# Performance work log

Hardware: AMD Instinct MI355X
Metric: run time of the kernel (lower is better)

The kernel has to match this reference:

```python
import jax, jax.numpy as jnp
import numpy as np
import math

WH, WW = 8, 8
N = WH * WW            # tokens per window = 64
DIM = 128
H = 4                  # num_heads
HD = DIM // H          # head_dim = 32
B_ = 3072              # num_windows * batch
NW = 192               # windows per image (96/8 * 128/8)
LAMBDA_INIT = 0.8 - 0.6 * math.exp(-0.3 * 0)  # layer_idx = 0 -> 0.2
EPS_RMS = 1e-9


def _polar_input():
    # Polar-coordinate relative positions, as in __init__
    gy, gx = jnp.meshgrid(jnp.arange(WH), jnp.arange(WW), indexing='ij')
    flat = jnp.stack([gy.reshape(-1), gx.reshape(-1)])          # (2, N)
    rel = flat[:, :, None] - flat[:, None, :]                   # (2, N, N)
    dx = rel[1].astype(jnp.float32)
    dy = -rel[0].astype(jnp.float32)
    r = jnp.sqrt(dx * dx + dy * dy + 1e-9)
    theta = jnp.arctan2(dx, dy)
    max_r = math.sqrt((WH - 1) ** 2 + (WW - 1) ** 2)
    return jnp.stack([r / max_r, (theta + math.pi) / (2 * math.pi)], axis=-1)  # (N, N, 2)


def setup_inputs() -> dict:
    key = jax.random.key(0)
    ks = jax.random.split(key, 16)
    s = 0.02
    inp = {}
    inp['x'] = jax.random.normal(ks[0], (B_, N, DIM), jnp.float32)
    inp['mask'] = jnp.zeros((NW, N, N), jnp.float32)
    inp['Wqkv'] = jax.random.normal(ks[1], (3 * DIM, DIM), jnp.float32) * s
    inp['bqkv'] = jnp.zeros((3 * DIM,), jnp.float32)
    inp['Wqkv2'] = jax.random.normal(ks[2], (2 * DIM, DIM), jnp.float32) * s
    inp['bqkv2'] = jnp.zeros((2 * DIM,), jnp.float32)
    inp['Wp1'] = jax.random.normal(ks[3], (64, 2), jnp.float32) * 0.1
    inp['bp1'] = jnp.zeros((64,), jnp.float32)
    inp['Wp2'] = jax.random.normal(ks[4], (H, 64), jnp.float32) * 0.1
    inp['bp2'] = jnp.zeros((H,), jnp.float32)
    inp['lambda_q1'] = jax.random.normal(ks[5], (HD // 2,), jnp.float32) * 0.1
    inp['lambda_k1'] = jax.random.normal(ks[6], (HD // 2,), jnp.float32) * 0.1
    inp['lambda_q2'] = jax.random.normal(ks[7], (HD // 2,), jnp.float32) * 0.1
    inp['lambda_k2'] = jax.random.normal(ks[8], (HD // 2,), jnp.float32) * 0.1
    inp['subln_w'] = jnp.ones((HD,), jnp.float32)
    inp['Wproj'] = jax.random.normal(ks[9], (DIM, DIM), jnp.float32) * s
    inp['bproj'] = jnp.zeros((DIM,), jnp.float32)
    return inp


def reference(x, mask, Wqkv, bqkv, Wqkv2, bqkv2, Wp1, bp1, Wp2, bp2,
              lambda_q1, lambda_k1, lambda_q2, lambda_k2, subln_w, Wproj, bproj):
    scale = HD ** -0.5
    # primary q, k, v
    qkv = (x @ Wqkv.T + bqkv).reshape(B_, N, 3, H, HD).transpose(2, 0, 3, 1, 4)
    q, k, v = qkv[0] * scale, qkv[1], qkv[2]        # (B_, H, N, HD)
    # secondary q2, k2 for differential attention
    qk2 = (x @ Wqkv2.T + bqkv2).reshape(B_, N, 2, H, HD).transpose(2, 0, 3, 1, 4)
    q2, k2 = qk2[0] * scale, qk2[1]

    attn = jnp.einsum('bhnd,bhmd->bhnm', q, k)      # (B_, H, N, N)
    attn2 = jnp.einsum('bhnd,bhmd->bhnm', q2, k2)

    lam = (jnp.exp(jnp.sum(lambda_q1 * lambda_k1))
           - jnp.exp(jnp.sum(lambda_q2 * lambda_k2)) + LAMBDA_INIT)

    # MLP-based polar relative position bias (exact erf GELU, as nn.GELU)
    pin = _polar_input().reshape(-1, 2)
    pb = jax.nn.gelu(pin @ Wp1.T + bp1, approximate=False) @ Wp2.T + bp2
    pb = pb.reshape(N, N, H).transpose(2, 0, 1)     # (H, N, N)

    attn = attn - lam * attn2 + pb[None]
    # window mask (0 / -inf), broadcast over batch and heads
    attn = attn.reshape(B_ // NW, NW, H, N, N) + mask[None, :, None]
    attn = jax.nn.softmax(attn.reshape(B_, H, N, N), axis=-1)

    o = jnp.einsum('bhnm,bhmd->bhnd', attn, v)      # (B_, H, N, HD)
    # post-attention RMSNorm over head_dim, then differential rescale
    o = o * jax.lax.rsqrt(jnp.mean(o * o, axis=-1, keepdims=True) + EPS_RMS) * subln_w
    o = (o * (1.0 - LAMBDA_INIT)).transpose(0, 2, 1, 3).reshape(B_, N, DIM)
    return o @ Wproj.T + bproj
```

## Files before the change

kernel.cpp:

```cpp
#include <hip/hip_runtime.h>
#include <math.h>

typedef __attribute__((ext_vector_type(8))) short bf16x8;
typedef __attribute__((ext_vector_type(4))) float f32x4;

#define NWMASK 192
#define SCALE_Q 0.17677669529663687f

__device__ __forceinline__ unsigned short f2bf(float f) {
  union { float f; unsigned u; } v; v.f = f;
  return (unsigned short)((v.u + 0x7fffu + ((v.u >> 16) & 1u)) >> 16);
}

__device__ __forceinline__ unsigned pkbf(float a, float b) {
#if defined(__has_builtin)
#if __has_builtin(__builtin_amdgcn_cvt_pk_bf16_f32)
  auto r = __builtin_amdgcn_cvt_pk_bf16_f32(a, b);
  union { decltype(r) v; unsigned u; } c; c.v = r; return c.u;
#else
  return (unsigned)f2bf(a) | ((unsigned)f2bf(b) << 16);
#endif
#else
  return (unsigned)f2bf(a) | ((unsigned)f2bf(b) << 16);
#endif
}

__device__ __forceinline__ void pack8s(unsigned short* dst, const float* src) {
  float4 lo = *(const float4*)(src);
  float4 hi = *(const float4*)(src + 4);
  uint4 pk;
  pk.x = pkbf(lo.x, lo.y); pk.y = pkbf(lo.z, lo.w);
  pk.z = pkbf(hi.x, hi.y); pk.w = pkbf(hi.z, hi.w);
  *(uint4*)dst = pk;
}

__global__ void prep_kernel(const float* __restrict__ Wqkv, const float* __restrict__ Wqkv2,
                            const float* __restrict__ Wproj,
                            const float* __restrict__ Wp1, const float* __restrict__ bp1,
                            const float* __restrict__ Wp2, const float* __restrict__ bp2,
                            const float* __restrict__ mask,
                            const float* __restrict__ lq1, const float* __restrict__ lk1,
                            const float* __restrict__ lq2, const float* __restrict__ lk2,
                            unsigned short* __restrict__ Wb, float* __restrict__ pbT,
                            float* __restrict__ maskT, float* __restrict__ lamOut) {
  int bid = blockIdx.x;
  if (bid < 48) {
    int gid = bid * 256 + threadIdx.x;
    int l15 = gid & 15, quad = (gid >> 4) & 3, ks = (gid >> 6) & 3, ft = gid >> 8;
    int row = ft * 16 + l15;
    const float* src = (row < 384) ? (Wqkv + (size_t)row * 128)
                     : (row < 640) ? (Wqkv2 + (size_t)(row - 384) * 128)
                                   : (Wproj + (size_t)(row - 640) * 128);
    pack8s(Wb + (size_t)gid * 8, src + ks * 32 + quad * 8);
  } else if (bid < 64) {
    int idx = (bid - 48) * 256 + threadIdx.x;
    int i = idx >> 6, j = idx & 63;
    float dx = (float)((i & 7) - (j & 7));
    float dy = -(float)((i >> 3) - (j >> 3));
    float r = sqrtf(dx*dx + dy*dy + 1e-9f);
    float theta = atan2f(dx, dy);
    float p0 = r * (1.0f / 9.899494936611665f);
    float p1 = (theta + 3.14159265358979323846f) * (1.0f / 6.283185307179586f);
    float a0 = 0.f, a1 = 0.f, a2 = 0.f, a3 = 0.f;
    for (int f = 0; f < 64; ++f) {
      float hpre = p0 * Wp1[2*f] + p1 * Wp1[2*f+1] + bp1[f];
      float g = 0.5f * hpre * (1.0f + erff(hpre * 0.70710678118654752f));
      a0 += Wp2[f]       * g;
      a1 += Wp2[64 + f]  * g;
      a2 += Wp2[128 + f] * g;
      a3 += Wp2[192 + f] * g;
    }
    int o = j * 64 + i;
    pbT[o]          = a0 + bp2[0];
    pbT[4096 + o]   = a1 + bp2[1];
    pbT[8192 + o]   = a2 + bp2[2];
    pbT[12288 + o]  = a3 + bp2[3];
    if (bid == 48 && threadIdx.x == 0) {
      float s1 = 0.f, s2 = 0.f;
      for (int k = 0; k < 16; ++k) { s1 += lq1[k]*lk1[k]; s2 += lq2[k]*lk2[k]; }
      lamOut[0] = expf(s1) - expf(s2) + 0.2f;
    }
  } else {
    __shared__ float tile[64][65];
    int wm = bid - 64;
    const float* src = mask + (size_t)wm * 4096;
#pragma unroll
    for (int u = 0; u < 4; ++u) {
      int o = u * 1024 + threadIdx.x * 4;
      float4 v = *(const float4*)(src + o);
      int r = o >> 6, c = o & 63;
      tile[r][c] = v.x; tile[r][c+1] = v.y; tile[r][c+2] = v.z; tile[r][c+3] = v.w;
    }
    __syncthreads();
    float* dst = maskT + (size_t)wm * 4096;
#pragma unroll
    for (int u = 0; u < 4; ++u) {
      int o = u * 1024 + threadIdx.x * 4;
      int c = o >> 6, r = o & 63;
      float4 v;
      v.x = tile[r][c]; v.y = tile[r+1][c]; v.z = tile[r+2][c]; v.w = tile[r+3][c];
      *(float4*)(dst + o) = v;
    }
  }
}

__global__ __launch_bounds__(256, 4)
void fused_win(const float* __restrict__ x, const unsigned short* __restrict__ Wb,
               const float* __restrict__ bqkv, const float* __restrict__ bqkv2,
               const float* __restrict__ lamBuf,
               const float* __restrict__ subln, const float* __restrict__ bproj,
               const float* __restrict__ pbT, const float* __restrict__ maskT,
               float* __restrict__ out) {
  __shared__ unsigned short smem[20480];

  const int b = blockIdx.x;
  const int t = threadIdx.x;
  const int w = t >> 6;
  const int lane = t & 63;
  const int l15 = lane & 15;
  const int quad = lane >> 4;
  const int h = w;
  const f32x4 zero4 = (f32x4){0.f, 0.f, 0.f, 0.f};
  const float lam = lamBuf[0];

  {
    const float* xg = x + (size_t)b * 8192;
#pragma unroll
    for (int u = 0; u < 4; ++u) {
      int id = u * 256 + t;
      int r = id >> 4, c16 = id & 15;
      pack8s(&smem[r * 128 + ((c16 ^ (r & 7)) * 8)], xg + r * 128 + c16 * 8);
    }
  }
  __syncthreads();

  unsigned short* AR = smem + 8192 + w * 3072;
  unsigned short* BR = AR + 2048;

  auto ldXB = [&](int mi, int ks) -> bf16x8 {
    int row = mi * 16 + l15;
    return *(const bf16x8*)(&smem[row * 128 + (((ks * 4 + quad) ^ (l15 & 7)) * 8)]);
  };
  auto ldWbF = [&](int ft, int ks) -> bf16x8 {
    return *(const bf16x8*)(Wb + ((((size_t)ft * 4 + ks) * 4 + quad) * 16 + l15) * 8);
  };

  auto proj2 = [&](int ft0, int ft1, f32x4 (&acc)[4][2]) {
#pragma unroll
    for (int mi = 0; mi < 4; ++mi) { acc[mi][0] = zero4; acc[mi][1] = zero4; }
#pragma unroll
    for (int ks = 0; ks < 4; ++ks) {
      bf16x8 w0 = ldWbF(ft0, ks), w1 = ldWbF(ft1, ks);
      bf16x8 xa[4];
#pragma unroll
      for (int mi = 0; mi < 4; ++mi) xa[mi] = ldXB(mi, ks);
      __builtin_amdgcn_s_setprio(1);
#pragma unroll
      for (int mi = 0; mi < 4; ++mi) {
        acc[mi][0] = __builtin_amdgcn_mfma_f32_16x16x32_bf16(xa[mi], w0, acc[mi][0], 0, 0, 0);
        acc[mi][1] = __builtin_amdgcn_mfma_f32_16x16x32_bf16(xa[mi], w1, acc[mi][1], 0, 0, 0);
      }
      __builtin_amdgcn_s_setprio(0);
    }
  };
  auto storeQ = [&](f32x4 (&acc)[4][2], const float* bias, float sc) {
#pragma unroll
    for (int nj = 0; nj < 2; ++nj) {
      int c32 = nj * 16 + l15;
      float bv = bias[c32];
      int g = c32 >> 3, c7 = c32 & 7;
#pragma unroll
      for (int mi = 0; mi < 4; ++mi) {
        f32x4 a = acc[mi][nj];
        unsigned p01 = pkbf((a[0] + bv) * sc, (a[1] + bv) * sc);
        unsigned p23 = pkbf((a[2] + bv) * sc, (a[3] + bv) * sc);
        int r0 = mi * 16 + quad * 4;
        AR[(r0+0) * 32 + ((g ^ ((r0+0) & 3)) * 8) + c7] = (unsigned short)p01;
        AR[(r0+1) * 32 + ((g ^ ((r0+1) & 3)) * 8) + c7] = (unsigned short)(p01 >> 16);
        AR[(r0+2) * 32 + ((g ^ ((r0+2) & 3)) * 8) + c7] = (unsigned short)p23;
        AR[(r0+3) * 32 + ((g ^ ((r0+3) & 3)) * 8) + c7] = (unsigned short)(p23 >> 16);
      }
    }
  };
  auto storeKh = [&](f32x4 (&acc)[4][2], int miBase, const float* bias) {
#pragma unroll
    for (int nj = 0; nj < 2; ++nj) {
      int c32 = nj * 16 + l15;
      float bv = bias[c32];
      int g = c32 >> 3, c7 = c32 & 7;
#pragma unroll
      for (int mi = 0; mi < 2; ++mi) {
        f32x4 a = acc[miBase + mi][nj];
        unsigned p01 = pkbf(a[0] + bv, a[1] + bv);
        unsigned p23 = pkbf(a[2] + bv, a[3] + bv);
        int r0 = mi * 16 + quad * 4;
        BR[(r0+0) * 32 + ((g ^ ((r0+0) & 3)) * 8) + c7] = (unsigned short)p01;
        BR[(r0+1) * 32 + ((g ^ ((r0+1) & 3)) * 8) + c7] = (unsigned short)(p01 >> 16);
        BR[(r0+2) * 32 + ((g ^ ((r0+2) & 3)) * 8) + c7] = (unsigned short)p23;
        BR[(r0+3) * 32 + ((g ^ ((r0+3) & 3)) * 8) + c7] = (unsigned short)(p23 >> 16);
      }
    }
  };
  auto qkHalf = [&](f32x4 (&S)[4][4], int half, bool seed) {
    bf16x8 qa[4], kb[2];
#pragma unroll
    for (int mi = 0; mi < 4; ++mi) {
      int row = mi * 16 + l15;
      qa[mi] = *(const bf16x8*)(&AR[row * 32 + ((quad ^ (l15 & 3)) * 8)]);
    }
#pragma unroll
    for (int j = 0; j < 2; ++j) {
      int row = j * 16 + l15;
      kb[j] = *(const bf16x8*)(&BR[row * 32 + ((quad ^ (l15 & 3)) * 8)]);
    }
    const float* pbh = pbT + h * 4096;
    const float* mkh = maskT + (size_t)(b % NWMASK) * 4096;
    __builtin_amdgcn_s_setprio(1);
#pragma unroll
    for (int mi = 0; mi < 4; ++mi)
#pragma unroll
      for (int j = 0; j < 2; ++j) {
        int ni = half * 2 + j;
        f32x4 c;
        if (seed) {
          int off = (ni * 16 + l15) * 64 + mi * 16 + quad * 4;
          float4 p4 = *(const float4*)(pbh + off);
          float4 m4 = *(const float4*)(mkh + off);
          c[0] = p4.x + m4.x; c[1] = p4.y + m4.y;
          c[2] = p4.z + m4.z; c[3] = p4.w + m4.w;
        } else c = S[mi][ni];
        S[mi][ni] = __builtin_amdgcn_mfma_f32_16x16x32_bf16(qa[mi], kb[j], c, 0, 0, 0);
      }
    __builtin_amdgcn_s_setprio(0);
  };
  auto storePh = [&](unsigned (&pe)[4][4]) {
#pragma unroll
    for (int mi = 0; mi < 4; ++mi)
#pragma unroll
      for (int reg = 0; reg < 4; ++reg) {
        int row = mi * 16 + quad * 4 + reg;
        unsigned short* prow = AR + row * 32;
        int sw = row & 3;
        unsigned v = pe[mi][reg];
        prow[(((l15 >> 3) + 0) ^ sw) * 8 + (l15 & 7)] = (unsigned short)v;
        prow[(((l15 >> 3) + 2) ^ sw) * 8 + (l15 & 7)] = (unsigned short)(v >> 16);
      }
  };
  auto storeVh = [&](f32x4 (&av)[4][2], int miBase, const float* bias) {
#pragma unroll
    for (int nd = 0; nd < 2; ++nd) {
      int d = nd * 16 + l15;
      float bv = bias[d];
#pragma unroll
      for (int mi = 0; mi < 2; ++mi) {
        f32x4 a = av[miBase + mi][nd];
        int tok0 = mi * 16 + quad * 4;
        uint2 pk;
        pk.x = pkbf(a[0] + bv, a[1] + bv);
        pk.y = pkbf(a[2] + bv, a[3] + bv);
        *(uint2*)(&BR[d * 32 + ((((tok0 >> 3) ^ (d & 3))) * 8) + (tok0 & 7)]) = pk;
      }
    }
  };
  auto pvHalf = [&](f32x4 (&O)[4][2]) {
    bf16x8 pa[4], vb[2];
#pragma unroll
    for (int mi = 0; mi < 4; ++mi) {
      int row = mi * 16 + l15;
      pa[mi] = *(const bf16x8*)(&AR[row * 32 + ((quad ^ (l15 & 3)) * 8)]);
    }
#pragma unroll
    for (int nd = 0; nd < 2; ++nd) {
      int d = nd * 16 + l15;
      vb[nd] = *(const bf16x8*)(&BR[d * 32 + ((quad ^ (l15 & 3)) * 8)]);
    }
    __builtin_amdgcn_s_setprio(1);
#pragma unroll
    for (int mi = 0; mi < 4; ++mi) {
      O[mi][0] = __builtin_amdgcn_mfma_f32_16x16x32_bf16(pa[mi], vb[0], O[mi][0], 0, 0, 0);
      O[mi][1] = __builtin_amdgcn_mfma_f32_16x16x32_bf16(pa[mi], vb[1], O[mi][1], 0, 0, 0);
    }
    __builtin_amdgcn_s_setprio(0);
  };

  f32x4 S[4][4];
  {
    f32x4 acc[4][2];
    proj2(24 + 2*h, 25 + 2*h, acc);
    storeQ(acc, bqkv2 + h*32, -lam * SCALE_Q);
    proj2(32 + 2*h, 33 + 2*h, acc);
    storeKh(acc, 0, bqkv2 + 128 + h*32);
    qkHalf(S, 0, true);
    storeKh(acc, 2, bqkv2 + 128 + h*32);
    qkHalf(S, 1, true);
  }
  {
    f32x4 acc[4][2];
    proj2(2*h, 1 + 2*h, acc);
    storeQ(acc, bqkv + h*32, SCALE_Q);
    proj2(8 + 2*h, 9 + 2*h, acc);
    storeKh(acc, 0, bqkv + 128 + h*32);
    qkHalf(S, 0, false);
    storeKh(acc, 2, bqkv + 128 + h*32);
    qkHalf(S, 1, false);
  }

  unsigned pe01[4][4], pe23[4][4];
#pragma unroll
  for (int mi = 0; mi < 4; ++mi)
#pragma unroll
    for (int reg = 0; reg < 4; ++reg) {
      pe01[mi][reg] = pkbf(__expf(S[mi][0][reg]), __expf(S[mi][1][reg]));
      pe23[mi][reg] = pkbf(__expf(S[mi][2][reg]), __expf(S[mi][3][reg]));
    }
  storePh(pe01);

  f32x4 av[4][2];
  proj2(16 + 2*h, 17 + 2*h, av);

  __syncthreads();

  float ov0[4][4], ov1[4][4];
  {
    const float* vbias = bqkv + 256 + h * 32;
    f32x4 O[4][2];
#pragma unroll
    for (int mi = 0; mi < 4; ++mi) { O[mi][0] = zero4; O[mi][1] = zero4; }
    storeVh(av, 0, vbias);
    pvHalf(O);
    storePh(pe23);
    storeVh(av, 2, vbias);
    pvHalf(O);

    float sw0 = subln[l15] * 0.8f;
    float sw1 = subln[16 + l15] * 0.8f;
#pragma unroll
    for (int mi = 0; mi < 4; ++mi)
#pragma unroll
      for (int reg = 0; reg < 4; ++reg) {
        float a0 = O[mi][0][reg], a1 = O[mi][1][reg];
        float ss = a0 * a0 + a1 * a1;
        ss += __shfl_xor(ss, 1);
        ss += __shfl_xor(ss, 2);
        ss += __shfl_xor(ss, 4);
        ss += __shfl_xor(ss, 8);
        float rs = 1.0f / sqrtf(ss * (1.0f / 32.0f));
        ov0[mi][reg] = a0 * rs * sw0;
        ov1[mi][reg] = a1 * rs * sw1;
      }
  }

  {
    int c0 = h * 32 + l15, c1 = h * 32 + 16 + l15;
#pragma unroll
    for (int mi = 0; mi < 4; ++mi)
#pragma unroll
      for (int reg = 0; reg < 4; ++reg) {
        int row = mi * 16 + quad * 4 + reg;
        unsigned short* orow = smem + row * 128;
        unsigned p = pkbf(ov0[mi][reg], ov1[mi][reg]);
        orow[(((c0 >> 3) ^ (row & 7)) * 8) + (c0 & 7)] = (unsigned short)p;
        orow[(((c1 >> 3) ^ (row & 7)) * 8) + (c1 & 7)] = (unsigned short)(p >> 16);
      }
  }
  __syncthreads();

  {
    f32x4 po[4][2];
#pragma unroll
    for (int mi = 0; mi < 4; ++mi) { po[mi][0] = zero4; po[mi][1] = zero4; }
#pragma unroll
    for (int ks = 0; ks < 4; ++ks) {
      bf16x8 oa[4];
#pragma unroll
      for (int mi = 0; mi < 4; ++mi) {
        int row = mi * 16 + l15;
        oa[mi] = *(const bf16x8*)(&smem[row * 128 + (((ks * 4 + quad) ^ (l15 & 7)) * 8)]);
      }
      bf16x8 w0 = ldWbF(40 + 2*w, ks), w1 = ldWbF(41 + 2*w, ks);
      __builtin_amdgcn_s_setprio(1);
#pragma unroll
      for (int mi = 0; mi < 4; ++mi) {
        po[mi][0] = __builtin_amdgcn_mfma_f32_16x16x32_bf16(oa[mi], w0, po[mi][0], 0, 0, 0);
        po[mi][1] = __builtin_amdgcn_mfma_f32_16x16x32_bf16(oa[mi], w1, po[mi][1], 0, 0, 0);
      }
      __builtin_amdgcn_s_setprio(0);
    }
    float* og = out + (size_t)b * 8192;
#pragma unroll
    for (int nt = 0; nt < 2; ++nt) {
      int col = (2 * w + nt) * 16 + l15;
      float bp = bproj[col];
#pragma unroll
      for (int mi = 0; mi < 4; ++mi)
#pragma unroll
        for (int reg = 0; reg < 4; ++reg)
          og[(size_t)(mi * 16 + quad * 4 + reg) * 128 + col] = po[mi][nt][reg] + bp;
    }
  }
}

extern "C" void kernel_launch(void* const* d_in, const int* in_sizes, int n_in,
                              void* d_out, int out_size, void* d_ws, size_t ws_size,
                              hipStream_t stream) {
  (void)in_sizes; (void)n_in; (void)out_size; (void)ws_size;
  const float* x     = (const float*)d_in[0];
  const float* mask  = (const float*)d_in[1];
  const float* Wqkv  = (const float*)d_in[2];
  const float* bqkv  = (const float*)d_in[3];
  const float* Wqkv2 = (const float*)d_in[4];
  const float* bqkv2 = (const float*)d_in[5];
  const float* Wp1   = (const float*)d_in[6];
  const float* bp1   = (const float*)d_in[7];
  const float* Wp2   = (const float*)d_in[8];
  const float* bp2   = (const float*)d_in[9];
  const float* lq1   = (const float*)d_in[10];
  const float* lk1   = (const float*)d_in[11];
  const float* lq2   = (const float*)d_in[12];
  const float* lk2   = (const float*)d_in[13];
  const float* subln = (const float*)d_in[14];
  const float* Wproj = (const float*)d_in[15];
  const float* bproj = (const float*)d_in[16];
  float* out = (float*)d_out;

  unsigned short* Wb = (unsigned short*)d_ws;
  float* lamBuf = (float*)((char*)d_ws + 200704);
  float* pbT   = (float*)((char*)d_ws + 262144);
  float* maskT = (float*)((char*)d_ws + 327680);

  hipLaunchKernelGGL(prep_kernel, dim3(256), dim3(256), 0, stream,
                     Wqkv, Wqkv2, Wproj, Wp1, bp1, Wp2, bp2, mask,
                     lq1, lk1, lq2, lk2, Wb, pbT, maskT, lamBuf);
  hipLaunchKernelGGL(fused_win, dim3(3072), dim3(256), 0, stream,
                     x, Wb, bqkv, bqkv2, lamBuf, subln, bproj,
                     pbT, maskT, out);
}
```

Measured before the change: 338.3 us.

## Split each head across two waves by token rows, doubling block to 512 threads

The fused window kernel now uses 8 waves per block instead of 4. Each head is handled by two waves, each owning 32 of the 64 query/token rows. Q/K/V/P are shared per head through LDS with extra block barriers. Each wave's register tiles are halved, which raises occupancy and parallelism per window. The cost is more __syncthreads, a larger LDS footprint, and duplicated weight-fragment loads across the paired waves.

```diff
diff --git a/kernel.cpp b/kernel.cpp
--- a/kernel.cpp
+++ b/kernel.cpp
@@ -104,238 +104,215 @@
   }
 }
 
-__global__ __launch_bounds__(256, 4)
+__global__ __launch_bounds__(512, 6)
 void fused_win(const float* __restrict__ x, const unsigned short* __restrict__ Wb,
                const float* __restrict__ bqkv, const float* __restrict__ bqkv2,
                const float* __restrict__ lamBuf,
                const float* __restrict__ subln, const float* __restrict__ bproj,
                const float* __restrict__ pbT, const float* __restrict__ maskT,
                float* __restrict__ out) {
-  __shared__ unsigned short smem[20480];
+  __shared__ unsigned short smem[24576];
 
   const int b = blockIdx.x;
   const int t = threadIdx.x;
   const int w = t >> 6;
+  const int h = w >> 1;
+  const int m = w & 1;
   const int lane = t & 63;
   const int l15 = lane & 15;
   const int quad = lane >> 4;
-  const int h = w;
+  const int Rb = m * 32;
   const f32x4 zero4 = (f32x4){0.f, 0.f, 0.f, 0.f};
   const float lam = lamBuf[0];
 
   {
     const float* xg = x + (size_t)b * 8192;
 #pragma unroll
-    for (int u = 0; u < 4; ++u) {
-      int id = u * 256 + t;
+    for (int u = 0; u < 2; ++u) {
+      int id = u * 512 + t;
       int r = id >> 4, c16 = id & 15;
       pack8s(&smem[r * 128 + ((c16 ^ (r & 7)) * 8)], xg + r * 128 + c16 * 8);
     }
   }
   __syncthreads();
 
-  unsigned short* AR = smem + 8192 + w * 3072;
-  unsigned short* BR = AR + 2048;
+  unsigned short* QB = smem + 8192 + h * 4096;
+  unsigned short* KB = QB + 2048;
+  unsigned short* PB = QB;
+  unsigned short* VT = smem + h * 2048;
 
   auto ldXB = [&](int mi, int ks) -> bf16x8 {
-    int row = mi * 16 + l15;
+    int row = Rb + mi * 16 + l15;
     return *(const bf16x8*)(&smem[row * 128 + (((ks * 4 + quad) ^ (l15 & 7)) * 8)]);
   };
   auto ldWbF = [&](int ft, int ks) -> bf16x8 {
     return *(const bf16x8*)(Wb + ((((size_t)ft * 4 + ks) * 4 + quad) * 16 + l15) * 8);
   };
 
-  auto proj2 = [&](int ft0, int ft1, f32x4 (&acc)[4][2]) {
-#pragma unroll
-    for (int mi = 0; mi < 4; ++mi) { acc[mi][0] = zero4; acc[mi][1] = zero4; }
+  auto proj2h = [&](int ft0, int ft1, f32x4 (&acc)[2][2]) {
+#pragma unroll
+    for (int mi = 0; mi < 2; ++mi) { acc[mi][0] = zero4; acc[mi][1] = zero4; }
 #pragma unroll
     for (int ks = 0; ks < 4; ++ks) {
       bf16x8 w0 = ldWbF(ft0, ks), w1 = ldWbF(ft1, ks);
-      bf16x8 xa[4];
-#pragma unroll
-      for (int mi = 0; mi < 4; ++mi) xa[mi] = ldXB(mi, ks);
+      bf16x8 xa[2];
+#pragma unroll
+      for (int mi = 0; mi < 2; ++mi) xa[mi] = ldXB(mi, ks);
       __builtin_amdgcn_s_setprio(1);
 #pragma unroll
-      for (int mi = 0; mi < 4; ++mi) {
+      for (int mi = 0; mi < 2; ++mi) {
         acc[mi][0] = __builtin_amdgcn_mfma_f32_16x16x32_bf16(xa[mi], w0, acc[mi][0], 0, 0, 0);
         acc[mi][1] = __builtin_amdgcn_mfma_f32_16x16x32_bf16(xa[mi], w1, acc[mi][1], 0, 0, 0);
       }
       __builtin_amdgcn_s_setprio(0);
     }
   };
-  auto storeQ = [&](f32x4 (&acc)[4][2], const float* bias, float sc) {
+  auto storeM32 = [&](unsigned short* buf, f32x4 (&acc)[2][2], const float* bias, float sc) {
 #pragma unroll
     for (int nj = 0; nj < 2; ++nj) {
       int c32 = nj * 16 + l15;
       float bv = bias[c32];
       int g = c32 >> 3, c7 = c32 & 7;
 #pragma unroll
-      for (int mi = 0; mi < 4; ++mi) {
+      for (int mi = 0; mi < 2; ++mi) {
         f32x4 a = acc[mi][nj];
         unsigned p01 = pkbf((a[0] + bv) * sc, (a[1] + bv) * sc);
         unsigned p23 = pkbf((a[2] + bv) * sc, (a[3] + bv) * sc);
-        int r0 = mi * 16 + quad * 4;
-        AR[(r0+0) * 32 + ((g ^ ((r0+0) & 3)) * 8) + c7] = (unsigned short)p01;
-        AR[(r0+1) * 32 + ((g ^ ((r0+1) & 3)) * 8) + c7] = (unsigned short)(p01 >> 16);
-        AR[(r0+2) * 32 + ((g ^ ((r0+2) & 3)) * 8) + c7] = (unsigned short)p23;
-        AR[(r0+3) * 32 + ((g ^ ((r0+3) & 3)) * 8) + c7] = (unsigned short)(p23 >> 16);
+        int r0 = Rb + mi * 16 + quad * 4;
+        buf[(r0+0) * 32 + ((g ^ ((r0+0) & 3)) * 8) + c7] = (unsigned short)p01;
+        buf[(r0+1) * 32 + ((g ^ ((r0+1) & 3)) * 8) + c7] = (unsigned short)(p01 >> 16);
+        buf[(r0+2) * 32 + ((g ^ ((r0+2) & 3)) * 8) + c7] = (unsigned short)p23;
+        buf[(r0+3) * 32 + ((g ^ ((r0+3) & 3)) * 8) + c7] = (unsigned short)(p23 >> 16);
       }
     }
   };
-  auto storeKh = [&](f32x4 (&acc)[4][2], int miBase, const float* bias) {
-#pragma unroll
-    for (int nj = 0; nj < 2; ++nj) {
-      int c32 = nj * 16 + l15;
-      float bv = bias[c32];
-      int g = c32 >> 3, c7 = c32 & 7;
-#pragma unroll
-      for (int mi = 0; mi < 2; ++mi) {
-        f32x4 a = acc[miBase + mi][nj];
-        unsigned p01 = pkbf(a[0] + bv, a[1] + bv);
-        unsigned p23 = pkbf(a[2] + bv, a[3] + bv);
-        int r0 = mi * 16 + quad * 4;
-        BR[(r0+0) * 32 + ((g ^ ((r0+0) & 3)) * 8) + c7] = (unsigned short)p01;
-        BR[(r0+1) * 32 + ((g ^ ((r0+1) & 3)) * 8) + c7] = (unsigned short)(p01 >> 16);
-        BR[(r0+2) * 32 + ((g ^ ((r0+2) & 3)) * 8) + c7] = (unsigned short)p23;
-        BR[(r0+3) * 32 + ((g ^ ((r0+3) & 3)) * 8) + c7] = (unsigned short)(p23 >> 16);
-      }
-    }
-  };
-  auto qkHalf = [&](f32x4 (&S)[4][4], int half, bool seed) {
-    bf16x8 qa[4], kb[2];
-#pragma unroll
-    for (int mi = 0; mi < 4; ++mi) {
-      int row = mi * 16 + l15;
-      qa[mi] = *(const bf16x8*)(&AR[row * 32 + ((quad ^ (l15 & 3)) * 8)]);
-    }
-#pragma unroll
-    for (int j = 0; j < 2; ++j) {
-      int row = j * 16 + l15;
-      kb[j] = *(const bf16x8*)(&BR[row * 32 + ((quad ^ (l15 & 3)) * 8)]);
+  auto qkAll = [&](f32x4 (&S)[2][4], bool seed) {
+    bf16x8 qa[2], kb[4];
+#pragma unroll
+    for (int mi = 0; mi < 2; ++mi) {
+      int row = Rb + mi * 16 + l15;
+      qa[mi] = *(const bf16x8*)(&QB[row * 32 + ((quad ^ (l15 & 3)) * 8)]);
+    }
+#pragma unroll
+    for (int ni = 0; ni < 4; ++ni) {
+      int row = ni * 16 + l15;
+      kb[ni] = *(const bf16x8*)(&KB[row * 32 + ((quad ^ (l15 & 3)) * 8)]);
     }
     const float* pbh = pbT + h * 4096;
     const float* mkh = maskT + (size_t)(b % NWMASK) * 4096;
     __builtin_amdgcn_s_setprio(1);
 #pragma unroll
-    for (int mi = 0; mi < 4; ++mi)
-#pragma unroll
-      for (int j = 0; j < 2; ++j) {
-        int ni = half * 2 + j;
+    for (int mi = 0; mi < 2; ++mi)
+#pragma unroll
+      for (int ni = 0; ni < 4; ++ni) {
         f32x4 c;
         if (seed) {
-          int off = (ni * 16 + l15) * 64 + mi * 16 + quad * 4;
+          int off = (ni * 16 + l15) * 64 + Rb + mi * 16 + quad * 4;
           float4 p4 = *(const float4*)(pbh + off);
           float4 m4 = *(const float4*)(mkh + off);
           c[0] = p4.x + m4.x; c[1] = p4.y + m4.y;
           c[2] = p4.z + m4.z; c[3] = p4.w + m4.w;
         } else c = S[mi][ni];
-        S[mi][ni] = __builtin_amdgcn_mfma_f32_16x16x32_bf16(qa[mi], kb[j], c, 0, 0, 0);
+        S[mi][ni] = __builtin_amdgcn_mfma_f32_16x16x32_bf16(qa[mi], kb[ni], c, 0, 0, 0);
       }
     __builtin_amdgcn_s_setprio(0);
   };
-  auto storePh = [&](unsigned (&pe)[4][4]) {
-#pragma unroll
-    for (int mi = 0; mi < 4; ++mi)
-#pragma unroll
-      for (int reg = 0; reg < 4; ++reg) {
-        int row = mi * 16 + quad * 4 + reg;
-        unsigned short* prow = AR + row * 32;
-        int sw = row & 3;
-        unsigned v = pe[mi][reg];
-        prow[(((l15 >> 3) + 0) ^ sw) * 8 + (l15 & 7)] = (unsigned short)v;
-        prow[(((l15 >> 3) + 2) ^ sw) * 8 + (l15 & 7)] = (unsigned short)(v >> 16);
-      }
-  };
-  auto storeVh = [&](f32x4 (&av)[4][2], int miBase, const float* bias) {
-#pragma unroll
-    for (int nd = 0; nd < 2; ++nd) {
-      int d = nd * 16 + l15;
-      float bv = bias[d];
-#pragma unroll
-      for (int mi = 0; mi < 2; ++mi) {
-        f32x4 a = av[miBase + mi][nd];
-        int tok0 = mi * 16 + quad * 4;
-        uint2 pk;
-        pk.x = pkbf(a[0] + bv, a[1] + bv);
-        pk.y = pkbf(a[2] + bv, a[3] + bv);
-        *(uint2*)(&BR[d * 32 + ((((tok0 >> 3) ^ (d & 3))) * 8) + (tok0 & 7)]) = pk;
-      }
-    }
-  };
-  auto pvHalf = [&](f32x4 (&O)[4][2]) {
-    bf16x8 pa[4], vb[2];
-#pragma unroll
-    for (int mi = 0; mi < 4; ++mi) {
-      int row = mi * 16 + l15;
-      pa[mi] = *(const bf16x8*)(&AR[row * 32 + ((quad ^ (l15 & 3)) * 8)]);
-    }
-#pragma unroll
-    for (int nd = 0; nd < 2; ++nd) {
-      int d = nd * 16 + l15;
-      vb[nd] = *(const bf16x8*)(&BR[d * 32 + ((quad ^ (l15 & 3)) * 8)]);
-    }
-    __builtin_amdgcn_s_setprio(1);
-#pragma unroll
-    for (int mi = 0; mi < 4; ++mi) {
-      O[mi][0] = __builtin_amdgcn_mfma_f32_16x16x32_bf16(pa[mi], vb[0], O[mi][0], 0, 0, 0);
-      O[mi][1] = __builtin_amdgcn_mfma_f32_16x16x32_bf16(pa[mi], vb[1], O[mi][1], 0, 0, 0);
-    }
-    __builtin_amdgcn_s_setprio(0);
-  };
-
-  f32x4 S[4][4];
-  {
-    f32x4 acc[4][2];
-    proj2(24 + 2*h, 25 + 2*h, acc);
-    storeQ(acc, bqkv2 + h*32, -lam * SCALE_Q);
-    proj2(32 + 2*h, 33 + 2*h, acc);
-    storeKh(acc, 0, bqkv2 + 128 + h*32);
-    qkHalf(S, 0, true);
-    storeKh(acc, 2, bqkv2 + 128 + h*32);
-    qkHalf(S, 1, true);
-  }
-  {
-    f32x4 acc[4][2];
-    proj2(2*h, 1 + 2*h, acc);
-    storeQ(acc, bqkv + h*32, SCALE_Q);
-    proj2(8 + 2*h, 9 + 2*h, acc);
-    storeKh(acc, 0, bqkv + 128 + h*32);
-    qkHalf(S, 0, false);
-    storeKh(acc, 2, bqkv + 128 + h*32);
-    qkHalf(S, 1, false);
-  }
-
-  unsigned pe01[4][4], pe23[4][4];
-#pragma unroll
-  for (int mi = 0; mi < 4; ++mi)
+
+  f32x4 S[2][4];
+  {
+    f32x4 acc[2][2];
+    proj2h(24 + 2*h, 25 + 2*h, acc);
+    storeM32(QB, acc, bqkv2 + h*32, -lam * SCALE_Q);
+    proj2h(32 + 2*h, 33 + 2*h, acc);
+    storeM32(KB, acc, bqkv2 + 128 + h*32, 1.0f);
+  }
+  __syncthreads();
+  qkAll(S, true);
+  __syncthreads();
+  {
+    f32x4 acc[2][2];
+    proj2h(2*h, 1 + 2*h, acc);
+    storeM32(QB, acc, bqkv + h*32, SCALE_Q);
+    proj2h(8 + 2*h, 9 + 2*h, acc);
+    storeM32(KB, acc, bqkv + 128 + h*32, 1.0f);
+  }
+  __syncthreads();
+  qkAll(S, false);
+
+  unsigned pe01[2][4], pe23[2][4];
+#pragma unroll
+  for (int mi = 0; mi < 2; ++mi)
 #pragma unroll
     for (int reg = 0; reg < 4; ++reg) {
       pe01[mi][reg] = pkbf(__expf(S[mi][0][reg]), __expf(S[mi][1][reg]));
       pe23[mi][reg] = pkbf(__expf(S[mi][2][reg]), __expf(S[mi][3][reg]));
     }
-  storePh(pe01);
-
-  f32x4 av[4][2];
-  proj2(16 + 2*h, 17 + 2*h, av);
-
-  __syncthreads();
-
-  float ov0[4][4], ov1[4][4];
+  __syncthreads();
+#pragma unroll
+  for (int mi = 0; mi < 2; ++mi)
+#pragma unroll
+    for (int reg = 0; reg < 4; ++reg) {
+      int row = Rb + mi * 16 + quad * 4 + reg;
+      unsigned short* prow = PB + row * 64;
+      int sw = row & 7;
+      unsigned v01 = pe01[mi][reg], v23 = pe23[mi][reg];
+      prow[(((l15 >> 3) + 0) ^ sw) * 8 + (l15 & 7)] = (unsigned short)v01;
+      prow[(((l15 >> 3) + 2) ^ sw) * 8 + (l15 & 7)] = (unsigned short)(v01 >> 16);
+      prow[(((l15 >> 3) + 4) ^ sw) * 8 + (l15 & 7)] = (unsigned short)v23;
+      prow[(((l15 >> 3) + 6) ^ sw) * 8 + (l15 & 7)] = (unsigned short)(v23 >> 16);
+    }
+
+  f32x4 av[2][2];
+  proj2h(16 + 2*h, 17 + 2*h, av);
+  __syncthreads();
   {
     const float* vbias = bqkv + 256 + h * 32;
-    f32x4 O[4][2];
-#pragma unroll
-    for (int mi = 0; mi < 4; ++mi) { O[mi][0] = zero4; O[mi][1] = zero4; }
-    storeVh(av, 0, vbias);
-    pvHalf(O);
-    storePh(pe23);
-    storeVh(av, 2, vbias);
-    pvHalf(O);
-
+#pragma unroll
+    for (int nd = 0; nd < 2; ++nd) {
+      int d = nd * 16 + l15;
+      float bv = vbias[d];
+#pragma unroll
+      for (int mi = 0; mi < 2; ++mi) {
+        int tok = Rb + mi * 16 + quad * 4;
+        uint2 pk;
+        pk.x = pkbf(av[mi][nd][0] + bv, av[mi][nd][1] + bv);
+        pk.y = pkbf(av[mi][nd][2] + bv, av[mi][nd][3] + bv);
+        *(uint2*)(&VT[d * 64 + (((tok >> 3) ^ (d & 7)) * 8) + (tok & 7)]) = pk;
+      }
+    }
+  }
+  __syncthreads();
+
+  float ov0[2][4], ov1[2][4];
+  {
+    f32x4 O[2][2];
+#pragma unroll
+    for (int mi = 0; mi < 2; ++mi) { O[mi][0] = zero4; O[mi][1] = zero4; }
+#pragma unroll
+    for (int kc = 0; kc < 2; ++kc) {
+      bf16x8 pa[2], vb[2];
+#pragma unroll
+      for (int mi = 0; mi < 2; ++mi) {
+        int row = Rb + mi * 16 + l15;
+        pa[mi] = *(const bf16x8*)(&PB[row * 64 + (((kc * 4 + quad) ^ (row & 7)) * 8)]);
+      }
+#pragma unroll
+      for (int nd = 0; nd < 2; ++nd) {
+        int d = nd * 16 + l15;
+        vb[nd] = *(const bf16x8*)(&VT[d * 64 + (((kc * 4 + quad) ^ (d & 7)) * 8)]);
+      }
+      __builtin_amdgcn_s_setprio(1);
+#pragma unroll
+      for (int mi = 0; mi < 2; ++mi) {
+        O[mi][0] = __builtin_amdgcn_mfma_f32_16x16x32_bf16(pa[mi], vb[0], O[mi][0], 0, 0, 0);
+        O[mi][1] = __builtin_amdgcn_mfma_f32_16x16x32_bf16(pa[mi], vb[1], O[mi][1], 0, 0, 0);
+      }
+      __builtin_amdgcn_s_setprio(0);
+    }
     float sw0 = subln[l15] * 0.8f;
     float sw1 = subln[16 + l15] * 0.8f;
 #pragma unroll
-    for (int mi = 0; mi < 4; ++mi)
+    for (int mi = 0; mi < 2; ++mi)
 #pragma unroll
       for (int reg = 0; reg < 4; ++reg) {
         float a0 = O[mi][0][reg], a1 = O[mi][1][reg];
@@ -349,15 +326,17 @@
         ov1[mi][reg] = a1 * rs * sw1;
       }
   }
-
-  {
+  __syncthreads();
+
+  {
+    unsigned short* OB = smem + 8192;
     int c0 = h * 32 + l15, c1 = h * 32 + 16 + l15;
 #pragma unroll
-    for (int mi = 0; mi < 4; ++mi)
+    for (int mi = 0; mi < 2; ++mi)
 #pragma unroll
       for (int reg = 0; reg < 4; ++reg) {
-        int row = mi * 16 + quad * 4 + reg;
-        unsigned short* orow = smem + row * 128;
+        int row = Rb + mi * 16 + quad * 4 + reg;
+        unsigned short* orow = OB + row * 128;
         unsigned p = pkbf(ov0[mi][reg], ov1[mi][reg]);
         orow[(((c0 >> 3) ^ (row & 7)) * 8) + (c0 & 7)] = (unsigned short)p;
         orow[(((c1 >> 3) ^ (row & 7)) * 8) + (c1 & 7)] = (unsigned short)(p >> 16);
@@ -366,21 +345,22 @@
   __syncthreads();
 
   {
-    f32x4 po[4][2];
-#pragma unroll
-    for (int mi = 0; mi < 4; ++mi) { po[mi][0] = zero4; po[mi][1] = zero4; }
+    unsigned short* OB = smem + 8192;
+    f32x4 po[2][2];
+#pragma unroll
+    for (int mi = 0; mi < 2; ++mi) { po[mi][0] = zero4; po[mi][1] = zero4; }
 #pragma unroll
     for (int ks = 0; ks < 4; ++ks) {
-      bf16x8 oa[4];
-#pragma unroll
-      for (int mi = 0; mi < 4; ++mi) {
-        int row = mi * 16 + l15;
-        oa[mi] = *(const bf16x8*)(&smem[row * 128 + (((ks * 4 + quad) ^ (l15 & 7)) * 8)]);
-      }
-      bf16x8 w0 = ldWbF(40 + 2*w, ks), w1 = ldWbF(41 + 2*w, ks);
+      bf16x8 oa[2];
+#pragma unroll
+      for (int mi = 0; mi < 2; ++mi) {
+        int row = Rb + mi * 16 + l15;
+        oa[mi] = *(const bf16x8*)(&OB[row * 128 + (((ks * 4 + quad) ^ (l15 & 7)) * 8)]);
+      }
+      bf16x8 w0 = ldWbF(40 + 2*h, ks), w1 = ldWbF(41 + 2*h, ks);
       __builtin_amdgcn_s_setprio(1);
 #pragma unroll
-      for (int mi = 0; mi < 4; ++mi) {
+      for (int mi = 0; mi < 2; ++mi) {
         po[mi][0] = __builtin_amdgcn_mfma_f32_16x16x32_bf16(oa[mi], w0, po[mi][0], 0, 0, 0);
         po[mi][1] = __builtin_amdgcn_mfma_f32_16x16x32_bf16(oa[mi], w1, po[mi][1], 0, 0, 0);
       }
@@ -389,13 +369,13 @@
     float* og = out + (size_t)b * 8192;
 #pragma unroll
     for (int nt = 0; nt < 2; ++nt) {
-      int col = (2 * w + nt) * 16 + l15;
+      int col = h * 32 + nt * 16 + l15;
       float bp = bproj[col];
 #pragma unroll
-      for (int mi = 0; mi < 4; ++mi)
+      for (int mi = 0; mi < 2; ++mi)
 #pragma unroll
         for (int reg = 0; reg < 4; ++reg)
-          og[(size_t)(mi * 16 + quad * 4 + reg) * 128 + col] = po[mi][nt][reg] + bp;
+          og[(size_t)(Rb + mi * 16 + quad * 4 + reg) * 128 + col] = po[mi][nt][reg] + bp;
     }
   }
 }
@@ -431,7 +411,7 @@
   hipLaunchKernelGGL(prep_kernel, dim3(256), dim3(256), 0, stream,
                      Wqkv, Wqkv2, Wproj, Wp1, bp1, Wp2, bp2, mask,
                      lq1, lk1, lq2, lk2, Wb, pbT, maskT, lamBuf);
-  hipLaunchKernelGGL(fused_win, dim3(3072), dim3(256), 0, stream,
+  hipLaunchKernelGGL(fused_win, dim3(3072), dim3(512), 0, stream,
                      x, Wb, bqkv, bqkv2, lamBuf, subln, bproj,
                      pbT, maskT, out);
 }
```

After: 324.5 us. 1.04x faster.
